# Optimization experiments

Measured on AMD Instinct MI355X. Metric: run time of the kernel, lower is better.

## Reference

```python
import jax, jax.numpy as jnp
import numpy as np

H = 256  # hidden_size
D = 256  # in_vocab_size
T = 512  # sequence length


def setup_inputs() -> dict:
    key = jax.random.key(0)
    k1, k2, k3, k4, k5 = jax.random.split(key, 5)
    # faithful param init from the torch module
    u1 = jax.random.uniform(k1, (H,), minval=1e-4, maxval=1.0)
    u2 = jax.random.uniform(k2, (H,), minval=1e-4, maxval=1.0)
    lamda = jnp.log(-0.5 * jnp.log(u1))
    theta = jnp.log(6.28 * u2)
    B_c1 = jax.random.normal(k3, (H, D), dtype=jnp.float32) / np.float32(np.sqrt(D))
    B_c2 = jax.random.normal(k4, (H, D), dtype=jnp.float32) / np.float32(np.sqrt(D))
    x_sequence = jax.random.normal(k5, (T, D), dtype=jnp.float32)
    return {"x_sequence": x_sequence, "lamda": lamda, "theta": theta,
            "B_c1": B_c1, "B_c2": B_c2}


def reference(x_sequence, lamda, theta, B_c1, B_c2):
    Hh = lamda.shape[0]
    Dd = B_c1.shape[1]
    # per-step constant coefficients (depend only on params)
    y = jnp.exp(-jnp.exp(lamda))
    z = jnp.exp(theta)
    gamma = jnp.sqrt(1.0 - y * y)
    cz, sz = jnp.cos(z), jnp.sin(z)
    c, s = y * cz, y * sz                       # rotation coefficients [H]
    y_g = -jnp.exp(lamda) * y                   # dy/dlamda
    gamma_g = -y / gamma * y_g                  # dgamma/dlamda
    z_g = jnp.exp(theta)                        # dz/dtheta
    # precompute input projections for all steps: [T, H]
    Bx1 = x_sequence @ B_c1.T
    Bx2 = x_sequence @ B_c2.T

    def step(carry, xs):
        h1, h2, sr1, sr2, st1, st2, sB11, sB12, sB21, sB22 = carry
        x_t, bx1, bx2 = xs
        # hidden state (complex diagonal rotation, split into 2 real channels)
        h1n = c * h1 - s * h2 + gamma * bx1
        h2n = c * h2 + s * h1 + gamma * bx2
        # RTRL sensitivities w.r.t. lamda
        sr1n = y_g * cz * h1 + c * sr1 - y_g * sz * h2 - s * sr2 + gamma_g * bx1
        sr2n = y_g * cz * h2 + c * sr2 + y_g * sz * h1 + s * sr1 + gamma_g * bx2
        # RTRL sensitivities w.r.t. theta
        st1n = -s * z_g * h1 + c * st1 - c * z_g * h2 - s * st2
        st2n = -s * z_g * h2 + c * st2 + c * z_g * h1 + s * st1
        # RTRL sensitivities w.r.t. B matrices, [H, D]
        gx = gamma[:, None] * x_t[None, :]
        sB11n = c[:, None] * sB11 - s[:, None] * sB12 + gx
        sB12n = c[:, None] * sB12 + s[:, None] * sB11
        sB21n = c[:, None] * sB21 - s[:, None] * sB22
        sB22n = c[:, None] * sB22 + s[:, None] * sB21 + gx
        out = jnp.concatenate([h1n, h2n])       # [2H]
        return (h1n, h2n, sr1n, sr2n, st1n, st2n, sB11n, sB12n, sB21n, sB22n), out

    zv = jnp.zeros((Hh,), jnp.float32)
    zm = jnp.zeros((Hh, Dd), jnp.float32)
    init = (zv, zv, zv, zv, zv, zv, zm, zm, zm, zm)
    _, outs = jax.lax.scan(step, init, (x_sequence, Bx1, Bx2))
    return outs  # [T, 2H]
```

## Files before the change

### kernel.cpp

```cpp
#include <hip/hip_runtime.h>

#define TT 512
#define DD 256
#define HH 256
#define CC 64
#define LL (TT / CC)

__device__ inline void coeffs(const float* __restrict__ lamda,
                              const float* __restrict__ theta, int j,
                              float& c, float& s, float& g) {
  const float y = __expf(-__expf(lamda[j]));
  const float z = __expf(theta[j]);
  c = y * __cosf(z);
  s = y * __sinf(z);
  g = sqrtf(fmaxf(1.0f - y * y, 0.0f));
}

__global__ __launch_bounds__(256) void rtu_chunk(
    const float* __restrict__ x, const float* __restrict__ lamda,
    const float* __restrict__ theta, const float* __restrict__ B1,
    const float* __restrict__ B2, float* __restrict__ out,
    float* __restrict__ E) {
  __shared__ float xs[LL][DD];
  const int cidx = blockIdx.x;
  const int t0 = cidx * LL;
  const int j = threadIdx.x;

  {
    const float4* xsrc = (const float4*)(x + t0 * DD);
    float4* xdst = (float4*)(&xs[0][0]);
    for (int i = j; i < LL * DD / 4; i += 256) xdst[i] = xsrc[i];
  }
  __syncthreads();

  const float4* b1 = (const float4*)(B1 + j * DD);
  const float4* b2 = (const float4*)(B2 + j * DD);
  const float4* xs4 = (const float4*)(&xs[0][0]);

  float a1[LL], a2[LL];
#pragma unroll
  for (int tt = 0; tt < LL; ++tt) { a1[tt] = 0.f; a2[tt] = 0.f; }

#pragma unroll 8
  for (int k4 = 0; k4 < DD / 4; ++k4) {
    float4 v1 = b1[k4];
    float4 v2 = b2[k4];
#pragma unroll
    for (int tt = 0; tt < LL; ++tt) {
      float4 xv = xs4[tt * (DD / 4) + k4];
      a1[tt] = fmaf(v1.x, xv.x, a1[tt]);
      a1[tt] = fmaf(v1.y, xv.y, a1[tt]);
      a1[tt] = fmaf(v1.z, xv.z, a1[tt]);
      a1[tt] = fmaf(v1.w, xv.w, a1[tt]);
      a2[tt] = fmaf(v2.x, xv.x, a2[tt]);
      a2[tt] = fmaf(v2.y, xv.y, a2[tt]);
      a2[tt] = fmaf(v2.z, xv.z, a2[tt]);
      a2[tt] = fmaf(v2.w, xv.w, a2[tt]);
    }
  }

  float c, s, g;
  coeffs(lamda, theta, j, c, s, g);

  float h1 = 0.f, h2 = 0.f;
#pragma unroll
  for (int tt = 0; tt < LL; ++tt) {
    const float bb1 = a1[tt] * g;
    const float bb2 = a2[tt] * g;
    const float n1 = fmaf(c, h1, fmaf(-s, h2, bb1));
    const float n2 = fmaf(c, h2, fmaf(s, h1, bb2));
    h1 = n1;
    h2 = n2;
    out[(t0 + tt) * (2 * HH) + j] = h1;
    out[(t0 + tt) * (2 * HH) + HH + j] = h2;
  }
  E[cidx * (2 * HH) + j] = h1;
  E[cidx * (2 * HH) + HH + j] = h2;
}

__global__ __launch_bounds__(256) void rtu_combine(
    const float* __restrict__ lamda, const float* __restrict__ theta,
    const float* __restrict__ E, float* __restrict__ carry) {
  const int j = threadIdx.x;
  float c, s, g;
  coeffs(lamda, theta, j, c, s, g);
  float cl = c, sl = s;
#pragma unroll
  for (int q = 0; q < 3; ++q) {
    const float nc = cl * cl - sl * sl;
    const float ns = 2.f * cl * sl;
    cl = nc;
    sl = ns;
  }
  float S1 = 0.f, S2 = 0.f;
#pragma unroll 16
  for (int ci = 0; ci < CC; ++ci) {
    carry[ci * (2 * HH) + j] = S1;
    carry[ci * (2 * HH) + HH + j] = S2;
    const float E1 = E[ci * (2 * HH) + j];
    const float E2 = E[ci * (2 * HH) + HH + j];
    const float n1 = fmaf(cl, S1, fmaf(-sl, S2, E1));
    const float n2 = fmaf(cl, S2, fmaf(sl, S1, E2));
    S1 = n1;
    S2 = n2;
  }
}

__global__ __launch_bounds__(256) void rtu_correct(
    const float* __restrict__ lamda, const float* __restrict__ theta,
    const float* __restrict__ carry, float* __restrict__ out) {
  const int cidx = blockIdx.x;
  const int t0 = cidx * LL;
  const int j = threadIdx.x;
  float c, s, g;
  coeffs(lamda, theta, j, c, s, g);
  const float S1 = carry[cidx * (2 * HH) + j];
  const float S2 = carry[cidx * (2 * HH) + HH + j];
  float p1 = c, p2 = s;
#pragma unroll
  for (int i = 0; i < LL; ++i) {
    const int t = t0 + i;
    const float o1 = out[t * (2 * HH) + j] + p1 * S1 - p2 * S2;
    const float o2 = out[t * (2 * HH) + HH + j] + p2 * S1 + p1 * S2;
    out[t * (2 * HH) + j] = o1;
    out[t * (2 * HH) + HH + j] = o2;
    const float np1 = p1 * c - p2 * s;
    const float np2 = p1 * s + p2 * c;
    p1 = np1;
    p2 = np2;
  }
}

extern "C" void kernel_launch(void* const* d_in, const int* in_sizes, int n_in,
                              void* d_out, int out_size, void* d_ws, size_t ws_size,
                              hipStream_t stream) {
  const float* x     = (const float*)d_in[0];
  const float* lamda = (const float*)d_in[1];
  const float* theta = (const float*)d_in[2];
  const float* B1    = (const float*)d_in[3];
  const float* B2    = (const float*)d_in[4];
  float* out = (float*)d_out;

  float* E = (float*)d_ws;
  float* carry = E + CC * 2 * HH;

  rtu_chunk<<<dim3(CC), 256, 0, stream>>>(x, lamda, theta, B1, B2, out, E);
  rtu_combine<<<1, 256, 0, stream>>>(lamda, theta, E, carry);
  rtu_correct<<<dim3(CC), 256, 0, stream>>>(lamda, theta, carry, out);
}
```

Before: 93.23 us.

## Merge carry combine into correction kernel and double chunk count

Each correction block now computes its own incoming carry by scanning the chunk end-states of all earlier chunks, which removes the single-block serial combine kernel and one launch. The number of chunks rises from 64 to 128, so each chunk covers 4 timesteps. This gives the first kernel more blocks and shortens each chunk's serial recurrence. In exchange, the carry work grows to a quadratic number of redundant reads of E across blocks, and the last block walks through 127 entries serially.

```diff
diff --git a/kernel.cpp b/kernel.cpp
--- a/kernel.cpp
+++ b/kernel.cpp
@@ -3,7 +3,7 @@
 #define TT 512
 #define DD 256
 #define HH 256
-#define CC 64
+#define CC 128
 #define LL (TT / CC)
 
 __device__ inline void coeffs(const float* __restrict__ lamda,
@@ -28,8 +28,7 @@
 
   {
     const float4* xsrc = (const float4*)(x + t0 * DD);
-    float4* xdst = (float4*)(&xs[0][0]);
-    for (int i = j; i < LL * DD / 4; i += 256) xdst[i] = xsrc[i];
+    ((float4*)(&xs[0][0]))[j] = xsrc[j];
   }
   __syncthreads();
 
@@ -78,44 +77,37 @@
   E[cidx * (2 * HH) + HH + j] = h2;
 }
 
-__global__ __launch_bounds__(256) void rtu_combine(
+__global__ __launch_bounds__(256) void rtu_fixup(
     const float* __restrict__ lamda, const float* __restrict__ theta,
-    const float* __restrict__ E, float* __restrict__ carry) {
+    const float* __restrict__ E, float* __restrict__ out) {
+  const int cidx = blockIdx.x;
+  if (cidx == 0) return;
   const int j = threadIdx.x;
   float c, s, g;
   coeffs(lamda, theta, j, c, s, g);
+
   float cl = c, sl = s;
 #pragma unroll
-  for (int q = 0; q < 3; ++q) {
+  for (int q = 0; q < 2; ++q) {
     const float nc = cl * cl - sl * sl;
     const float ns = 2.f * cl * sl;
     cl = nc;
     sl = ns;
   }
+
   float S1 = 0.f, S2 = 0.f;
-#pragma unroll 16
-  for (int ci = 0; ci < CC; ++ci) {
-    carry[ci * (2 * HH) + j] = S1;
-    carry[ci * (2 * HH) + HH + j] = S2;
-    const float E1 = E[ci * (2 * HH) + j];
-    const float E2 = E[ci * (2 * HH) + HH + j];
+  const float* Ep = E + j;
+#pragma unroll 8
+  for (int ci = 0; ci < cidx; ++ci) {
+    const float E1 = Ep[ci * (2 * HH)];
+    const float E2 = Ep[ci * (2 * HH) + HH];
     const float n1 = fmaf(cl, S1, fmaf(-sl, S2, E1));
     const float n2 = fmaf(cl, S2, fmaf(sl, S1, E2));
     S1 = n1;
     S2 = n2;
   }
-}
 
-__global__ __launch_bounds__(256) void rtu_correct(
-    const float* __restrict__ lamda, const float* __restrict__ theta,
-    const float* __restrict__ carry, float* __restrict__ out) {
-  const int cidx = blockIdx.x;
   const int t0 = cidx * LL;
-  const int j = threadIdx.x;
-  float c, s, g;
-  coeffs(lamda, theta, j, c, s, g);
-  const float S1 = carry[cidx * (2 * HH) + j];
-  const float S2 = carry[cidx * (2 * HH) + HH + j];
   float p1 = c, p2 = s;
 #pragma unroll
   for (int i = 0; i < LL; ++i) {
@@ -142,9 +134,7 @@
   float* out = (float*)d_out;
 
   float* E = (float*)d_ws;
-  float* carry = E + CC * 2 * HH;
 
   rtu_chunk<<<dim3(CC), 256, 0, stream>>>(x, lamda, theta, B1, B2, out, E);
-  rtu_combine<<<1, 256, 0, stream>>>(lamda, theta, E, carry);
-  rtu_correct<<<dim3(CC), 256, 0, stream>>>(lamda, theta, carry, out);
+  rtu_fixup<<<dim3(CC), 256, 0, stream>>>(lamda, theta, E, out);
 }
```

Measured after the change: 87.17 us. 6.5% less time.
